# Kernel tuning notes

Hardware: AMD Instinct MI355X
Metric: run time of the kernel (lower is better)

The kernel has to match this reference:

```python
import jax, jax.numpy as jnp
import numpy as np

EPS = 1e-5
K_NN = 16

def _lin1d(x, W, b):
    # 1x1 Conv1d: x (B,C,N) -> (B,O,N)
    return jnp.einsum('oc,bcn->bon', W, x) + b[None, :, None]

def _lin2d(x, W, b):
    # 1x1 Conv2d: x (B,C,N,K) -> (B,O,N,K)
    return jnp.einsum('oc,bcnk->bonk', W, x) + b[None, :, None, None]

def _bn2d(x, gamma, beta):
    # train-mode BatchNorm2d over (B, N, K) per channel
    mean = jnp.mean(x, axis=(0, 2, 3), keepdims=True)
    var = jnp.var(x, axis=(0, 2, 3), keepdims=True)
    xh = (x - mean) * jax.lax.rsqrt(var + EPS)
    return gamma[None, :, None, None] * xh + beta[None, :, None, None]

def _knn_idx(pq, ps, k):
    # pq (B,3,N), ps (B,3,M) -> idx (B,N,K) of k nearest support points
    d2 = (jnp.sum(pq * pq, axis=1)[:, :, None]
          + jnp.sum(ps * ps, axis=1)[:, None, :]
          - 2.0 * jnp.einsum('bcn,bcm->bnm', pq, ps))
    _, idx = jax.lax.top_k(-d2, k)
    return idx

def _group(x, idx):
    # x (B,C,M), idx (B,N,K) -> (B,C,N,K)
    return jnp.take_along_axis(x[:, :, None, :], idx[:, None, :, :], axis=3)

def setup_inputs() -> dict:
    key = jax.random.key(0)
    ks = jax.random.split(key, 20)
    B, C, D, N, M, H = 4, 128, 64, 2048, 2048, 256
    s = lambda k, shape, scale: (jax.random.normal(k, shape, dtype=jnp.float32) * scale)
    return {
        'pq': s(ks[0], (B, 3, N), 1.0),
        'fq': s(ks[1], (B, C, N), 1.0),
        'ps': s(ks[2], (B, 3, M), 1.0),
        'fs': s(ks[3], (B, C, M), 1.0),
        'Wq': s(ks[4], (D, C), 0.05), 'bq': jnp.zeros((D,), jnp.float32),
        'Wk': s(ks[5], (D, C), 0.05), 'bk': jnp.zeros((D,), jnp.float32),
        'Wv': s(ks[6], (D, C), 0.05), 'bv': jnp.zeros((D,), jnp.float32),
        'Wp1': s(ks[7], (D, 3), 0.2), 'bp1': jnp.zeros((D,), jnp.float32),
        'gp': jnp.ones((D,), jnp.float32), 'btp': jnp.zeros((D,), jnp.float32),
        'Wp2': s(ks[8], (D, D), 0.05), 'bp2': jnp.zeros((D,), jnp.float32),
        'Wa1': s(ks[9], (H, D), 0.05), 'ba1': jnp.zeros((H,), jnp.float32),
        'ga': jnp.ones((H,), jnp.float32), 'bta': jnp.zeros((H,), jnp.float32),
        'Wa2': s(ks[10], (D, H), 0.05), 'ba2': jnp.zeros((D,), jnp.float32),
        'We': s(ks[11], (C, D), 0.05), 'be': jnp.zeros((C,), jnp.float32),
    }

def reference(pq, fq, ps, fs, Wq, bq, Wk, bk, Wv, bv,
              Wp1, bp1, gp, btp, Wp2, bp2,
              Wa1, ba1, ga, bta, Wa2, ba2, We, be):
    identity = fq
    q = _lin1d(fq, Wq, bq)          # (B,D,N)
    k = _lin1d(fs, Wk, bk)          # (B,D,M)
    v = _lin1d(fs, Wv, bv)          # (B,D,M)
    idx = _knn_idx(pq, ps, K_NN)    # (B,N,K)
    key_g = _group(k, idx)          # (B,D,N,K)
    qk_rel = q[:, :, :, None] - key_g
    pos_rel = pq[:, :, :, None] - _group(ps, idx)  # (B,3,N,K)
    # pos_mlp: conv-bn-relu-conv
    pe = _lin2d(pos_rel, Wp1, bp1)
    pe = jax.nn.relu(_bn2d(pe, gp, btp))
    pe = _lin2d(pe, Wp2, bp2)       # (B,D,N,K)
    # attn_mlp: conv-bn-relu-conv
    a = _lin2d(qk_rel + pe, Wa1, ba1)
    a = jax.nn.relu(_bn2d(a, ga, bta))
    a = _lin2d(a, Wa2, ba2)         # (B,D,N,K)
    attn = jax.nn.softmax(a, axis=-1)
    val = _group(v, idx) + pe       # (B,D,N,K)
    agg = jnp.einsum('bcnk,bcnk->bcn', attn, val)
    return _lin1d(agg, We, be) + identity
```

## Files before the change

kernel.cpp:

```cpp
#include <hip/hip_runtime.h>
#include <stdint.h>

#define NN 2048
#define MM 2048
#define NSAMP 131072

typedef float  fv4 __attribute__((ext_vector_type(4)));
typedef short  bfv8 __attribute__((ext_vector_type(8)));
typedef short  bfv4 __attribute__((ext_vector_type(4)));
typedef unsigned short u16;
typedef unsigned long long u64;

__device__ inline u16 f2bf(float x){
  unsigned u = __float_as_uint(x);
  return (u16)((u + 0x7FFFu + ((u>>16)&1u)) >> 16);
}
__device__ inline float bf2f(u16 u){ return __uint_as_float(((unsigned)u)<<16); }
__device__ inline bfv8 ld8f(const float* __restrict__ p){
  fv4 a = *(const fv4*)p;
  fv4 b = *(const fv4*)(p + 4);
  bfv8 r;
  r[0]=(short)f2bf(a.x); r[1]=(short)f2bf(a.y); r[2]=(short)f2bf(a.z); r[3]=(short)f2bf(a.w);
  r[4]=(short)f2bf(b.x); r[5]=(short)f2bf(b.y); r[6]=(short)f2bf(b.z); r[7]=(short)f2bf(b.w);
  return r;
}
#define MFMA16 __builtin_amdgcn_mfma_f32_16x16x32_bf16

__global__ __launch_bounds__(256) void k_front(
    const float* __restrict__ fq, const float* __restrict__ fs,
    const float* __restrict__ Wq, const float* __restrict__ Wk, const float* __restrict__ Wv,
    const float* __restrict__ bq, const float* __restrict__ bk, const float* __restrict__ bv,
    const float* __restrict__ pq, const float* __restrict__ ps,
    float* __restrict__ qT, float* __restrict__ kT, float* __restrict__ vT,
    int* __restrict__ idxb, float* __restrict__ posPart) {
  __shared__ __align__(16) unsigned char smem[17408];
  const int t = threadIdx.x;

  if (blockIdx.x < 256) {
    u16* tile = (u16*)smem;
    int bid = blockIdx.x;
    int b = bid >> 6, p0 = (bid & 63) * 32;
    int w = t >> 6, l = t & 63, lq = l >> 4, ln = l & 15;
    {
      int cq = t >> 3, n4 = (t & 7) * 4;
      #pragma unroll
      for (int it = 0; it < 4; ++it) {
        int c = it * 32 + cq;
        fv4 vq = *(const fv4*)&fq[(b*128 + c)*2048 + p0 + n4];
        fv4 vs = *(const fv4*)&fs[(b*128 + c)*2048 + p0 + n4];
        #pragma unroll
        for (int j = 0; j < 4; ++j) {
          tile[0*32*136 + (n4 + j)*136 + c] = f2bf(vq[j]);
          tile[1*32*136 + (n4 + j)*136 + c] = f2bf(vs[j]);
        }
      }
    }
    bfv8 A[3][4];
    #pragma unroll
    for (int mat = 0; mat < 3; ++mat) {
      const float* W = mat == 0 ? Wq : (mat == 1 ? Wk : Wv);
      #pragma unroll
      for (int kk = 0; kk < 4; ++kk)
        A[mat][kk] = ld8f(W + (w*16 + ln)*128 + kk*32 + lq*8);
    }
    __syncthreads();
    fv4 acc[3][2];
    #pragma unroll
    for (int mat = 0; mat < 3; ++mat) {
      const u16* tl = tile + (mat == 0 ? 0 : 32*136);
      #pragma unroll
      for (int nt = 0; nt < 2; ++nt) {
        fv4 a = {0.f,0.f,0.f,0.f};
        #pragma unroll
        for (int kk = 0; kk < 4; ++kk) {
          bfv8 bb = *(const bfv8*)&tl[(nt*16 + ln)*136 + kk*32 + lq*8];
          a = MFMA16(A[mat][kk], bb, a, 0, 0, 0);
        }
        acc[mat][nt] = a;
      }
    }
    #pragma unroll
    for (int mat = 0; mat < 3; ++mat) {
      float* dst = mat == 0 ? qT : (mat == 1 ? kT : vT);
      const float* bia = mat == 0 ? bq : (mat == 1 ? bk : bv);
      fv4 bq4 = *(const fv4*)&bia[w*16 + lq*4];
      #pragma unroll
      for (int nt = 0; nt < 2; ++nt) {
        fv4 o = acc[mat][nt] + bq4;
        *(fv4*)&dst[(b*NN + p0 + nt*16 + ln)*64 + w*16 + lq*4] = o;
      }
    }
    return;
  }

  u64*   list = (u64*)smem;
  u64*   win  = (u64*)(smem + 16384);
  int*   cnt  = (int*)(smem + 16896);
  float* sacc = (float*)(smem + 16912);

  const int kbid = blockIdx.x - 256;
  const int w = t >> 6, lane = t & 63;
  const int qi = kbid * 4 + w;
  const int b = qi >> 11, n = qi & 2047;
  const float* pqb = pq + b * 3 * NN;
  const float* psb = ps + b * 3 * MM;
  const float qx = pqb[n], qy = pqb[NN + n], qz = pqb[2 * NN + n];
  const float qq = qx * qx + qy * qy + qz * qz;

  unsigned key[32];
  unsigned bkey = 0xFFFFFFFFu; unsigned bj = 0;
  #pragma unroll
  for (int j = 0; j < 32; ++j) {
    int m = lane + 64*j;
    float x = psb[m], y = psb[MM + m], z = psb[2*MM + m];
    float w2 = x*x + y*y + z*z;
    float d2 = qq + w2 - 2.f * (qx * x + qy * y + qz * z);
    unsigned bu = __float_as_uint(d2);
    bu = (bu & 0x80000000u) ? ~bu : (bu | 0x80000000u);
    key[j] = bu;
    if (bu < bkey) { bkey = bu; bj = (unsigned)j; }
  }
  u64 e = (((u64)bkey) << 32) | (unsigned)(lane + 64*(int)bj);

  #pragma unroll
  for (int k = 2; k <= 64; k <<= 1) {
    #pragma unroll
    for (int j = k >> 1; j > 0; j >>= 1) {
      u64 x = __shfl_xor(e, j, 64);
      u64 lo = e < x ? e : x, hi = e < x ? x : e;
      bool up = ((lane & k) == 0);
      bool takeLo = (((lane & j) == 0) == up);
      e = takeLo ? lo : hi;
    }
  }
  const u64 thr = __shfl(e, 15, 64);
  const unsigned T32 = (unsigned)(thr >> 32);

  if (lane == 0) cnt[w] = 0;
  #pragma unroll
  for (int j = 0; j < 32; ++j) {
    if (key[j] <= T32) {
      int p = atomicAdd(&cnt[w], 1);
      if (p < 512) list[w*512 + p] = (((u64)key[j]) << 32) | (unsigned)(lane + 64*j);
    }
  }
  const int C = *(volatile int*)&cnt[w];

  u64 myWin = 0;
  if (C <= 64) {
    u64 v = (lane < C) ? list[w*512 + lane] : ~0ULL;
    #pragma unroll
    for (int k = 2; k <= 64; k <<= 1) {
      #pragma unroll
      for (int j = k >> 1; j > 0; j >>= 1) {
        u64 x = __shfl_xor(v, j, 64);
        u64 lo = v < x ? v : x, hi = v < x ? x : v;
        bool up = ((lane & k) == 0);
        bool takeLo = (((lane & j) == 0) == up);
        v = takeLo ? lo : hi;
      }
    }
    myWin = v;
  } else if (C <= 128) {
    u64 e0 = list[w*512 + lane];
    u64 e1 = (64 + lane < C) ? list[w*512 + 64 + lane] : ~0ULL;
    #pragma unroll
    for (unsigned k = 2; k <= 128; k <<= 1) {
      #pragma unroll
      for (unsigned j = k >> 1; j > 0; j >>= 1) {
        if (j < 64) {
          u64 x0 = __shfl_xor(e0, (int)j, 64);
          u64 x1 = __shfl_xor(e1, (int)j, 64);
          bool lower = ((lane & j) == 0);
          bool up0 = (k == 128) ? true : ((lane & k) == 0);
          bool up1 = (k == 128) ? true : ((k == 64) ? false : ((lane & k) == 0));
          e0 = (lower == up0) ? (e0 < x0 ? e0 : x0) : (e0 < x0 ? x0 : e0);
          e1 = (lower == up1) ? (e1 < x1 ? e1 : x1) : (e1 < x1 ? x1 : e1);
        } else {
          u64 lo = e0 < e1 ? e0 : e1, hi = e0 < e1 ? e1 : e0;
          e0 = lo; e1 = hi;
        }
      }
    }
    myWin = e0;
  } else {
    int Cc = C > 512 ? 512 : C;
    for (int i = lane; i < 512; i += 64)
      if (i >= Cc) list[w*512 + i] = ~0ULL;
    for (int r = 0; r < 16; ++r) {
      u64 mv = ~0ULL;
      #pragma unroll
      for (int s5 = 0; s5 < 8; ++s5) {
        u64 x = list[w*512 + s5*64 + lane];
        mv = x < mv ? x : mv;
      }
      #pragma unroll
      for (int off = 1; off <= 32; off <<= 1) {
        u64 x = __shfl_xor(mv, off, 64);
        mv = x < mv ? x : mv;
      }
      #pragma unroll
      for (int s5 = 0; s5 < 8; ++s5)
        if (list[w*512 + s5*64 + lane] == mv) list[w*512 + s5*64 + lane] = ~0ULL;
      if (lane == 0) win[w*16 + r] = mv;
    }
    if (lane < 16) myWin = win[w*16 + lane];
  }

  if (lane < 16) {
    unsigned m = (unsigned)(myWin & 0xFFFFFFFFu);
    idxb[qi * 16 + lane] = (int)m;
    float x = psb[m], y = psb[MM + m], z = psb[2*MM + m];
    float r0 = qx - x, r1 = qy - y, r2 = qz - z;
    float s[9];
    s[0] = r0; s[1] = r1; s[2] = r2;
    s[3] = r0*r0; s[4] = r0*r1; s[5] = r0*r2;
    s[6] = r1*r1; s[7] = r1*r2; s[8] = r2*r2;
    #pragma unroll
    for (int off = 1; off <= 8; off <<= 1)
      #pragma unroll
      for (int i = 0; i < 9; ++i) s[i] += __shfl_xor(s[i], off, 64);
    if (lane == 0)
      #pragma unroll
      for (int i = 0; i < 9; ++i) sacc[w*9 + i] = s[i];
  }
  __syncthreads();
  if (t < 9) posPart[kbid * 12 + t]
      = sacc[0*9 + t] + sacc[1*9 + t] + sacc[2*9 + t] + sacc[3*9 + t];
}

__global__ __launch_bounds__(256) void k_ystats(
    const float* __restrict__ pq, const float* __restrict__ ps,
    const float* __restrict__ qT, const float* __restrict__ kT,
    const int* __restrict__ idxb, const float* __restrict__ posPart,
    const float* __restrict__ Wp1, const float* __restrict__ bp1,
    const float* __restrict__ gp, const float* __restrict__ btp,
    const float* __restrict__ Wp2, const float* __restrict__ bp2,
    float* __restrict__ Wp1f, float* __restrict__ bp1f,
    float* __restrict__ Gpart, float* __restrict__ ySumPart) {
  __shared__ __align__(16) unsigned char smem[21760];
  u16*   hp   = (u16*)smem;
  u16*   y2   = (u16*)(smem + 9216);
  float* r3   = (float*)(smem + 18432);
  float* qc   = (float*)(smem + 19200);
  int*   idxA = (int*)(smem + 20224);
  float* sWp1 = (float*)(smem + 20480);
  float* sbp1 = (float*)(smem + 21248);
  float* sbp2 = (float*)(smem + 21504);

  const int t = threadIdx.x;
  const int w = t >> 6, l = t & 63, lq = l >> 4, ln = l & 15;
  const int d0 = 16*w + lq*4;

  if (t < 64) sbp2[t] = bp2[t];

  bfv8 Ape[2];
  #pragma unroll
  for (int kk = 0; kk < 2; ++kk)
    Ape[kk] = ld8f(Wp2 + (16*w + ln)*64 + kk*32 + lq*8);

  {
    float* red = r3;
    float* stf = r3 + 40;
    float s[9];
    #pragma unroll
    for (int i = 0; i < 9; ++i) s[i] = 0.f;
    #pragma unroll
    for (int it = 0; it < 8; ++it) {
      const float* p = posPart + (it * 256 + t) * 12;
      fv4 a = *(const fv4*)p;
      fv4 b4 = *(const fv4*)(p + 4);
      float c8 = p[8];
      s[0]+=a.x; s[1]+=a.y; s[2]+=a.z; s[3]+=a.w;
      s[4]+=b4.x; s[5]+=b4.y; s[6]+=b4.z; s[7]+=b4.w;
      s[8]+=c8;
    }
    #pragma unroll
    for (int off = 32; off > 0; off >>= 1)
      #pragma unroll
      for (int i = 0; i < 9; ++i) s[i] += __shfl_xor(s[i], off, 64);
    if (l == 0)
      #pragma unroll
      for (int i = 0; i < 9; ++i) red[w*9 + i] = s[i];
    __syncthreads();
    if (t < 9) stf[t] = red[0*9+t] + red[1*9+t] + red[2*9+t] + red[3*9+t];
    __syncthreads();
    if (t < 64) {
      int d = t;
      const float invN = 1.f / (float)NSAMP;
      float m0 = stf[0]*invN, m1 = stf[1]*invN, m2 = stf[2]*invN;
      float C00 = stf[3]*invN - m0*m0, C01 = stf[4]*invN - m0*m1, C02 = stf[5]*invN - m0*m2;
      float C11 = stf[6]*invN - m1*m1, C12 = stf[7]*invN - m1*m2, C22 = stf[8]*invN - m2*m2;
      float w0 = Wp1[d*3], w1 = Wp1[d*3+1], w2 = Wp1[d*3+2];
      float mean = w0*m0 + w1*m1 + w2*m2 + bp1[d];
      float var = w0*w0*C00 + w1*w1*C11 + w2*w2*C22 + 2.f*(w0*w1*C01 + w0*w2*C02 + w1*w2*C12);
      float scale = gp[d] * rsqrtf(var + 1e-5f);
      float wf0 = scale * w0, wf1 = scale * w1, wf2 = scale * w2;
      float bf = btp[d] + scale * (bp1[d] - mean);
      sWp1[d*3] = wf0; sWp1[d*3+1] = wf1; sWp1[d*3+2] = wf2;
      sbp1[d] = bf;
      if (blockIdx.x == 0) {
        Wp1f[d*3] = wf0; Wp1f[d*3+1] = wf1; Wp1f[d*3+2] = wf2;
        bp1f[d] = bf;
      }
    }
  }

  fv4 gacc[4];
  #pragma unroll
  for (int nt = 0; nt < 4; ++nt) gacc[nt] = (fv4){0.f,0.f,0.f,0.f};
  float ys[4] = {0.f, 0.f, 0.f, 0.f};
  __syncthreads();

  for (int ch = 0; ch < 4; ++ch) {
    const int p0 = blockIdx.x * 16 + ch * 4;
    const int b  = p0 >> 11;
    const int bN = b * 2048;
    if (t < 64) idxA[t] = idxb[p0*16 + t];
    qc[t] = qT[(p0 + (t>>6))*64 + (t & 63)];
    __syncthreads();
    if (t < 192) { int c = t >> 6, s = t & 63; int n = (p0 + (s>>4)) & 2047;
      r3[c*64 + s] = pq[(b*3+c)*NN + n] - ps[(b*3+c)*MM + idxA[s]]; }
    __syncthreads();
    { int s = t >> 2, iq = t & 3;
      float r0 = r3[s], r1 = r3[64+s], r2 = r3[128+s];
      u16 tmp[16];
      #pragma unroll
      for (int e = 0; e < 16; ++e) { int i = iq*16 + e;
        float v = sbp1[i] + sWp1[i*3]*r0 + sWp1[i*3+1]*r1 + sWp1[i*3+2]*r2;
        tmp[e] = f2bf(fmaxf(v, 0.f)); }
      *(bfv8*)&hp[s*72 + iq*16]     = *(const bfv8*)&tmp[0];
      *(bfv8*)&hp[s*72 + iq*16 + 8] = *(const bfv8*)&tmp[8];
    }
    __syncthreads();
    {
      fv4 pe[4];
      #pragma unroll
      for (int nt = 0; nt < 4; ++nt) {
        fv4 acc = {0.f,0.f,0.f,0.f};
        #pragma unroll
        for (int kk = 0; kk < 2; ++kk) {
          bfv8 bb = *(const bfv8*)&hp[(nt*16 + ln)*72 + kk*32 + lq*8];
          acc = MFMA16(Ape[kk], bb, acc, 0, 0, 0);
        }
        pe[nt] = acc;
      }
      fv4 bp2q = *(const fv4*)&sbp2[d0];
      #pragma unroll
      for (int nt = 0; nt < 4; ++nt) {
        int s = nt*16 + ln;
        int mi = idxA[s];
        fv4 kg = *(const fv4*)(kT + (bN + mi)*64 + d0);
        fv4 qv = *(const fv4*)&qc[nt*64 + d0];
        fv4 yv = qv - kg + pe[nt] + bp2q;
        #pragma unroll
        for (int r = 0; r < 4; ++r) { y2[(d0 + r)*72 + s] = f2bf(yv[r]); ys[r] += yv[r]; }
      }
    }
    __syncthreads();
    #pragma unroll
    for (int kk = 0; kk < 2; ++kk) {
      bfv8 aa = *(const bfv8*)&y2[(16*w + ln)*72 + kk*32 + lq*8];
      #pragma unroll
      for (int nt = 0; nt < 4; ++nt) {
        bfv8 bb = *(const bfv8*)&y2[(nt*16 + ln)*72 + kk*32 + lq*8];
        gacc[nt] = MFMA16(aa, bb, gacc[nt], 0, 0, 0);
      }
    }
    __syncthreads();
  }
  #pragma unroll
  for (int nt = 0; nt < 4; ++nt)
    #pragma unroll
    for (int r = 0; r < 4; ++r)
      Gpart[blockIdx.x*4096 + (16*w + lq*4 + r)*64 + nt*16 + ln] = gacc[nt][r];
  #pragma unroll
  for (int off = 1; off <= 8; off <<= 1) {
    #pragma unroll
    for (int r = 0; r < 4; ++r) ys[r] += __shfl_xor(ys[r], off, 64);
  }
  if (ln == 0) {
    #pragma unroll
    for (int r = 0; r < 4; ++r) ySumPart[blockIdx.x*64 + d0 + r] = ys[r];
  }
}

__global__ __launch_bounds__(256) void k_gred(
    const float* __restrict__ Gpart, const float* __restrict__ ySumPart,
    float* __restrict__ G, float* __restrict__ ySum) {
  __shared__ float red[256];
  int bid = blockIdx.x, t = threadIdx.x;
  int tj = t & 63, st = t >> 6;
  if (bid < 64) {
    int j = bid * 64 + tj;
    float s = 0.f;
    for (int p = st * 128; p < st * 128 + 128; ++p)
      s += Gpart[p*4096 + j];
    red[st * 64 + tj] = s;
    __syncthreads();
    if (t < 64)
      G[bid * 64 + t] = red[t] + red[64 + t] + red[128 + t] + red[192 + t];
  } else {
    float s = 0.f;
    for (int p = st * 128; p < st * 128 + 128; ++p)
      s += ySumPart[p*64 + tj];
    red[st * 64 + tj] = s;
    __syncthreads();
    if (t < 64)
      ySum[t] = red[t] + red[64 + t] + red[128 + t] + red[192 + t];
  }
}

__global__ __launch_bounds__(256) void k_attnfinal(
    const float* __restrict__ Wa1, const float* __restrict__ ba1,
    const float* __restrict__ ga, const float* __restrict__ bta,
    const float* __restrict__ ySum, const float* __restrict__ G,
    u16* __restrict__ Wa1fbf, float* __restrict__ ba1f) {
  __shared__ float red[256];
  __shared__ float mu[64];
  __shared__ float sc[1];
  int h = blockIdx.x, t = threadIdx.x;
  const float invN = 1.f / (float)NSAMP;
  if (t < 64) mu[t] = ySum[t] * invN;
  __syncthreads();
  float acc = 0.f;
  #pragma unroll
  for (int e = 0; e < 16; ++e) {
    int pi = t*16 + e, i = pi >> 6, j = pi & 63;
    float cov = G[pi]*invN - mu[i]*mu[j];
    acc += Wa1[h*64 + i] * Wa1[h*64 + j] * cov;
  }
  red[t] = acc;
  __syncthreads();
  for (int s = 128; s > 0; s >>= 1) { if (t < s) red[t] += red[t + s]; __syncthreads(); }
  float var = red[0];
  __syncthreads();
  red[t] = (t < 64) ? Wa1[h*64 + t] * mu[t] : 0.f;
  __syncthreads();
  for (int s = 128; s > 0; s >>= 1) { if (t < s) red[t] += red[t + s]; __syncthreads(); }
  if (t == 0) {
    float mean  = red[0] + ba1[h];
    float scale = ga[h] * rsqrtf(var + 1e-5f);
    sc[0] = scale;
    ba1f[h] = bta[h] + scale * (ba1[h] - mean);
  }
  __syncthreads();
  if (t < 64) Wa1fbf[h*64 + t] = f2bf(sc[0] * Wa1[h*64 + t]);
}

__global__ __launch_bounds__(256) void k_main(
    const float* __restrict__ pq, const float* __restrict__ ps,
    const float* __restrict__ qT, const float* __restrict__ kT, const float* __restrict__ vT,
    const int* __restrict__ idxb,
    const float* __restrict__ Wp1f, const float* __restrict__ bp1f,
    const float* __restrict__ Wp2, const float* __restrict__ bp2,
    const u16* __restrict__ Wa1fbf, const float* __restrict__ ba1f,
    const float* __restrict__ Wa2, const float* __restrict__ ba2,
    const float* __restrict__ We, const float* __restrict__ be,
    const float* __restrict__ fq,
    u16* __restrict__ aggbf, float* __restrict__ out) {
  __shared__ __align__(16) unsigned char smem[65024];
  u16*   hp   = (u16*)smem;
  u16*   ha   = (u16*)smem;
  u16*   ylds = (u16*)(smem + 33792);
  float* at   = (float*)(smem + 33792);
  u16*   vt   = (u16*)(smem + 51200);
  float* r3   = (float*)(smem + 60416);
  float* qc   = (float*)(smem + 61184);
  int*   idxA = (int*)(smem + 62208);
  float* sWp1 = (float*)(smem + 62464);
  float* sbp1 = (float*)(smem + 63232);
  float* sbp2 = (float*)(smem + 63488);
  float* sba1 = (float*)(smem + 63744);
  float* sba2 = (float*)(smem + 64768);

  const int t = threadIdx.x;
  const int w = t >> 6, l = t & 63, lq = l >> 4, ln = l & 15;
  const int d0 = 16*w + lq*4;

  if (t < 192) sWp1[t] = Wp1f[t];
  if (t < 64){ sbp1[t] = bp1f[t]; sbp2[t] = bp2[t]; sba2[t] = ba2[t]; }
  sba1[t] = ba1f[t];

  bfv8 Ape[2], A1[4][2], A2[8];
  #pragma unroll
  for (int kk = 0; kk < 2; ++kk)
    Ape[kk] = ld8f(Wp2 + (16*w + ln)*64 + kk*32 + lq*8);
  #pragma unroll
  for (int mt = 0; mt < 4; ++mt)
    #pragma unroll
    for (int kk = 0; kk < 2; ++kk)
      A1[mt][kk] = *(const bfv8*)(Wa1fbf + (64*w + mt*16 + ln)*64 + kk*32 + lq*8);
  #pragma unroll
  for (int kk = 0; kk < 8; ++kk)
    A2[kk] = ld8f(Wa2 + (16*w + ln)*256 + kk*32 + lq*8);
  __syncthreads();

  for (int ch = 0; ch < 4; ++ch) {
    const int p0 = blockIdx.x * 16 + ch * 4;
    const int b  = p0 >> 11;
    const int bN = b * 2048;
    if (t < 64) idxA[t] = idxb[p0*16 + t];
    qc[t] = qT[(p0 + (t>>6))*64 + (t & 63)];
    __syncthreads();
    if (t < 192) { int c = t >> 6, s = t & 63; int n = (p0 + (s>>4)) & 2047;
      r3[c*64 + s] = pq[(b*3+c)*NN + n] - ps[(b*3+c)*MM + idxA[s]]; }
    __syncthreads();
    { int s = t >> 2, iq = t & 3;
      float r0 = r3[s], r1 = r3[64+s], r2 = r3[128+s];
      u16 tmp[16];
      #pragma unroll
      for (int e = 0; e < 16; ++e) { int i = iq*16 + e;
        float v = sbp1[i] + sWp1[i*3]*r0 + sWp1[i*3+1]*r1 + sWp1[i*3+2]*r2;
        tmp[e] = f2bf(fmaxf(v, 0.f)); }
      *(bfv8*)&hp[s*72 + iq*16]     = *(const bfv8*)&tmp[0];
      *(bfv8*)&hp[s*72 + iq*16 + 8] = *(const bfv8*)&tmp[8];
    }
    __syncthreads();
    {
      fv4 pe[4];
      #pragma unroll
      for (int nt = 0; nt < 4; ++nt) {
        fv4 acc = {0.f,0.f,0.f,0.f};
        #pragma unroll
        for (int kk = 0; kk < 2; ++kk) {
          bfv8 bb = *(const bfv8*)&hp[(nt*16 + ln)*72 + kk*32 + lq*8];
          acc = MFMA16(Ape[kk], bb, acc, 0, 0, 0);
        }
        pe[nt] = acc;
      }
      fv4 bp2q = *(const fv4*)&sbp2[d0];
      #pragma unroll
      for (int nt = 0; nt < 4; ++nt) {
        int s = nt*16 + ln;
        int mi = idxA[s];
        fv4 kg = *(const fv4*)(kT + (bN + mi)*64 + d0);
        fv4 vg = *(const fv4*)(vT + (bN + mi)*64 + d0);
        fv4 qv = *(const fv4*)&qc[nt*64 + d0];
        fv4 pv = pe[nt] + bp2q;
        fv4 yv = qv - kg + pv;
        fv4 vv = vg + pv;
        u16 yp[4], vp[4];
        #pragma unroll
        for (int r = 0; r < 4; ++r) { yp[r] = f2bf(yv[r]); vp[r] = f2bf(vv[r]); }
        *(bfv4*)&ylds[s*72 + d0] = *(const bfv4*)yp;
        *(bfv4*)&vt[s*72 + d0]   = *(const bfv4*)vp;
      }
    }
    __syncthreads();
    #pragma unroll
    for (int nt = 0; nt < 4; ++nt) {
      int s = nt*16 + ln;
      bfv8 b0 = *(const bfv8*)&ylds[s*72 + lq*8];
      bfv8 b1 = *(const bfv8*)&ylds[s*72 + 32 + lq*8];
      #pragma unroll
      for (int mt = 0; mt < 4; ++mt) {
        fv4 acc = {0.f,0.f,0.f,0.f};
        acc = MFMA16(A1[mt][0], b0, acc, 0, 0, 0);
        acc = MFMA16(A1[mt][1], b1, acc, 0, 0, 0);
        int h0 = 64*w + mt*16 + lq*4;
        fv4 bq = *(const fv4*)&sba1[h0];
        u16 hv[4];
        #pragma unroll
        for (int r = 0; r < 4; ++r) hv[r] = f2bf(fmaxf(acc[r] + bq[r], 0.f));
        *(bfv4*)&ha[s*264 + h0] = *(const bfv4*)hv;
      }
    }
    __syncthreads();
    {
      fv4 acc2[4];
      #pragma unroll
      for (int nt = 0; nt < 4; ++nt) acc2[nt] = (fv4){0.f,0.f,0.f,0.f};
      #pragma unroll
      for (int kk = 0; kk < 8; ++kk) {
        #pragma unroll
        for (int nt = 0; nt < 4; ++nt) {
          bfv8 bb = *(const bfv8*)&ha[(nt*16 + ln)*264 + kk*32 + lq*8];
          acc2[nt] = MFMA16(A2[kk], bb, acc2[nt], 0, 0, 0);
        }
      }
      fv4 ba2q = *(const fv4*)&sba2[d0];
      #pragma unroll
      for (int nt = 0; nt < 4; ++nt) {
        int s = nt*16 + ln;
        fv4 o = acc2[nt] + ba2q;
        *(fv4*)&at[s*68 + d0] = o;
      }
    }
    __syncthreads();
    {
      int dd = t & 63, pt = t >> 6;
      float a[16];
      #pragma unroll
      for (int k = 0; k < 16; ++k) a[k] = at[(pt*16 + k)*68 + dd];
      float mx = a[0];
      #pragma unroll
      for (int k = 1; k < 16; ++k) mx = fmaxf(mx, a[k]);
      float sum = 0.f, num = 0.f;
      #pragma unroll
      for (int k = 0; k < 16; ++k) {
        float e = __expf(a[k] - mx);
        sum += e;
        num += e * bf2f(vt[(pt*16 + k)*72 + dd]);
      }
      aggbf[(p0 + pt)*64 + dd] = f2bf(num / sum);
    }
    __syncthreads();
  }
  {
    const int P0 = blockIdx.x * 16;
    const int b  = P0 >> 11;
    const int n0 = P0 & 2047;
    bfv8 EA[2][2];
    #pragma unroll
    for (int mt = 0; mt < 2; ++mt)
      #pragma unroll
      for (int kk = 0; kk < 2; ++kk)
        EA[mt][kk] = ld8f(We + ((w*2 + mt)*16 + ln)*64 + kk*32 + lq*8);
    const u16* bp = aggbf + (P0 + ln)*64;
    bfv8 b0 = *(const bfv8*)(bp + lq*8);
    bfv8 b1 = *(const bfv8*)(bp + 32 + lq*8);
    fv4 eacc[2];
    #pragma unroll
    for (int mt = 0; mt < 2; ++mt) {
      fv4 a = {0.f,0.f,0.f,0.f};
      a = MFMA16(EA[mt][0], b0, a, 0, 0, 0);
      a = MFMA16(EA[mt][1], b1, a, 0, 0, 0);
      eacc[mt] = a;
    }
    #pragma unroll
    for (int mt = 0; mt < 2; ++mt) {
      int c0 = (w*2 + mt)*16 + lq*4;
      fv4 bev = *(const fv4*)&be[c0];
      #pragma unroll
      for (int r = 0; r < 4; ++r) {
        int c = c0 + r;
        int o = (b*128 + c)*2048 + n0 + ln;
        out[o] = eacc[mt][r] + bev[r] + fq[o];
      }
    }
  }
}

extern "C" void kernel_launch(void* const* d_in, const int* in_sizes, int n_in,
                              void* d_out, int out_size, void* d_ws, size_t ws_size,
                              hipStream_t stream) {
  (void)in_sizes; (void)n_in; (void)out_size; (void)ws_size;
  const float* pq  = (const float*)d_in[0];
  const float* fq  = (const float*)d_in[1];
  const float* ps  = (const float*)d_in[2];
  const float* fs  = (const float*)d_in[3];
  const float* Wq  = (const float*)d_in[4];  const float* bq  = (const float*)d_in[5];
  const float* Wk  = (const float*)d_in[6];  const float* bk  = (const float*)d_in[7];
  const float* Wv  = (const float*)d_in[8];  const float* bv  = (const float*)d_in[9];
  const float* Wp1 = (const float*)d_in[10]; const float* bp1 = (const float*)d_in[11];
  const float* gp  = (const float*)d_in[12]; const float* btp = (const float*)d_in[13];
  const float* Wp2 = (const float*)d_in[14]; const float* bp2 = (const float*)d_in[15];
  const float* Wa1 = (const float*)d_in[16]; const float* ba1 = (const float*)d_in[17];
  const float* ga  = (const float*)d_in[18]; const float* bta = (const float*)d_in[19];
  const float* Wa2 = (const float*)d_in[20]; const float* ba2 = (const float*)d_in[21];
  const float* We  = (const float*)d_in[22]; const float* be  = (const float*)d_in[23];
  float* ws = (float*)d_ws;
  float* qT    = ws;
  float* kT    = ws + 524288;
  float* vT    = ws + 1048576;
  u16*   aggbf = (u16*)(ws + 1572864);
  int*   idxb  = (int*)(ws + 1835008);
  float* Wp1f  = ws + 1998848;
  float* bp1f  = ws + 1999040;
  float* ba1f  = ws + 1999104;
  float* G     = ws + 1999360;
  float* ySum  = ws + 2003456;
  float* ySumP = ws + 2003520;
  u16*   Wa1fbf = (u16*)(ws + 2036288);
  float* posPart = ws + 2044480;
  float* Gpart   = ws + 2069056;
  float* out   = (float*)d_out;

  k_front<<<2304, 256, 0, stream>>>(fq, fs, Wq, Wk, Wv, bq, bk, bv, pq, ps,
                                    qT, kT, vT, idxb, posPart);
  k_ystats<<<512, 256, 0, stream>>>(pq, ps, qT, kT, idxb, posPart,
                                    Wp1, bp1, gp, btp, Wp2, bp2,
                                    Wp1f, bp1f, Gpart, ySumP);
  k_gred<<<65, 256, 0, stream>>>(Gpart, ySumP, G, ySum);
  k_attnfinal<<<256, 256, 0, stream>>>(Wa1, ba1, ga, bta, ySum, G, Wa1fbf, ba1f);
  k_main<<<512, 256, 0, stream>>>(pq, ps, qT, kT, vT, idxb, Wp1f, bp1f, Wp2, bp2,
                                  Wa1fbf, ba1f, Wa2, ba2, We, be, fq, aggbf, out);
}
```

Measured before the change: 208.6 us.

## Compute attn BN stats directly from Wa1·y instead of covariance Gram matrix

The ystats kernel now multiplies each tile of y by Wa1 with MFMA and accumulates per-channel sums and sums of squares of the 256 pre-BN attention channels. This replaces the 64x64 Gram-matrix partials, so the k_gred reduction kernel and the covariance contraction in k_attnfinal go away. That removes one launch and the large Gpart write and read traffic, at the cost of more MFMA work and registers in ystats. The variance now comes from E[a²]-E[a]² over bf16 MFMA outputs, which may change numerical accuracy.

```diff
diff --git a/kernel.cpp b/kernel.cpp
--- a/kernel.cpp
+++ b/kernel.cpp
@@ -236,11 +236,12 @@
     const float* __restrict__ Wp1, const float* __restrict__ bp1,
     const float* __restrict__ gp, const float* __restrict__ btp,
     const float* __restrict__ Wp2, const float* __restrict__ bp2,
+    const float* __restrict__ Wa1,
     float* __restrict__ Wp1f, float* __restrict__ bp1f,
-    float* __restrict__ Gpart, float* __restrict__ ySumPart) {
+    float* __restrict__ aSumP, float* __restrict__ aSqP) {
   __shared__ __align__(16) unsigned char smem[21760];
   u16*   hp   = (u16*)smem;
-  u16*   y2   = (u16*)(smem + 9216);
+  u16*   ylds = (u16*)(smem + 9216);
   float* r3   = (float*)(smem + 18432);
   float* qc   = (float*)(smem + 19200);
   int*   idxA = (int*)(smem + 20224);
@@ -254,10 +255,15 @@
 
   if (t < 64) sbp2[t] = bp2[t];
 
-  bfv8 Ape[2];
+  bfv8 Ape[2], A1[4][2];
   #pragma unroll
   for (int kk = 0; kk < 2; ++kk)
     Ape[kk] = ld8f(Wp2 + (16*w + ln)*64 + kk*32 + lq*8);
+  #pragma unroll
+  for (int mt = 0; mt < 4; ++mt)
+    #pragma unroll
+    for (int kk = 0; kk < 2; ++kk)
+      A1[mt][kk] = ld8f(Wa1 + (64*w + mt*16 + ln)*64 + kk*32 + lq*8);
 
   {
     float* red = r3;
@@ -306,10 +312,9 @@
     }
   }
 
-  fv4 gacc[4];
-  #pragma unroll
-  for (int nt = 0; nt < 4; ++nt) gacc[nt] = (fv4){0.f,0.f,0.f,0.f};
-  float ys[4] = {0.f, 0.f, 0.f, 0.f};
+  float aS[16], aQ[16];
+  #pragma unroll
+  for (int i = 0; i < 16; ++i) { aS[i] = 0.f; aQ[i] = 0.f; }
   __syncthreads();
 
   for (int ch = 0; ch < 4; ++ch) {
@@ -353,93 +358,74 @@
         fv4 kg = *(const fv4*)(kT + (bN + mi)*64 + d0);
         fv4 qv = *(const fv4*)&qc[nt*64 + d0];
         fv4 yv = qv - kg + pe[nt] + bp2q;
-        #pragma unroll
-        for (int r = 0; r < 4; ++r) { y2[(d0 + r)*72 + s] = f2bf(yv[r]); ys[r] += yv[r]; }
-      }
-    }
-    __syncthreads();
-    #pragma unroll
-    for (int kk = 0; kk < 2; ++kk) {
-      bfv8 aa = *(const bfv8*)&y2[(16*w + ln)*72 + kk*32 + lq*8];
-      #pragma unroll
-      for (int nt = 0; nt < 4; ++nt) {
-        bfv8 bb = *(const bfv8*)&y2[(nt*16 + ln)*72 + kk*32 + lq*8];
-        gacc[nt] = MFMA16(aa, bb, gacc[nt], 0, 0, 0);
-      }
-    }
-    __syncthreads();
-  }
-  #pragma unroll
-  for (int nt = 0; nt < 4; ++nt)
-    #pragma unroll
-    for (int r = 0; r < 4; ++r)
-      Gpart[blockIdx.x*4096 + (16*w + lq*4 + r)*64 + nt*16 + ln] = gacc[nt][r];
-  #pragma unroll
-  for (int off = 1; off <= 8; off <<= 1) {
-    #pragma unroll
-    for (int r = 0; r < 4; ++r) ys[r] += __shfl_xor(ys[r], off, 64);
-  }
+        u16 yp[4];
+        #pragma unroll
+        for (int r = 0; r < 4; ++r) yp[r] = f2bf(yv[r]);
+        *(bfv4*)&ylds[s*72 + d0] = *(const bfv4*)yp;
+      }
+    }
+    __syncthreads();
+    #pragma unroll
+    for (int nt = 0; nt < 4; ++nt) {
+      int s = nt*16 + ln;
+      bfv8 yb0 = *(const bfv8*)&ylds[s*72 + lq*8];
+      bfv8 yb1 = *(const bfv8*)&ylds[s*72 + 32 + lq*8];
+      #pragma unroll
+      for (int mt = 0; mt < 4; ++mt) {
+        fv4 acc = {0.f,0.f,0.f,0.f};
+        acc = MFMA16(A1[mt][0], yb0, acc, 0, 0, 0);
+        acc = MFMA16(A1[mt][1], yb1, acc, 0, 0, 0);
+        #pragma unroll
+        for (int r = 0; r < 4; ++r) {
+          float a = acc[r];
+          aS[mt*4 + r] += a;
+          aQ[mt*4 + r] += a * a;
+        }
+      }
+    }
+    __syncthreads();
+  }
+  #pragma unroll
+  for (int off = 1; off <= 8; off <<= 1)
+    #pragma unroll
+    for (int i = 0; i < 16; ++i) {
+      aS[i] += __shfl_xor(aS[i], off, 16);
+      aQ[i] += __shfl_xor(aQ[i], off, 16);
+    }
   if (ln == 0) {
     #pragma unroll
-    for (int r = 0; r < 4; ++r) ySumPart[blockIdx.x*64 + d0 + r] = ys[r];
-  }
-}
-
-__global__ __launch_bounds__(256) void k_gred(
-    const float* __restrict__ Gpart, const float* __restrict__ ySumPart,
-    float* __restrict__ G, float* __restrict__ ySum) {
-  __shared__ float red[256];
-  int bid = blockIdx.x, t = threadIdx.x;
-  int tj = t & 63, st = t >> 6;
-  if (bid < 64) {
-    int j = bid * 64 + tj;
-    float s = 0.f;
-    for (int p = st * 128; p < st * 128 + 128; ++p)
-      s += Gpart[p*4096 + j];
-    red[st * 64 + tj] = s;
-    __syncthreads();
-    if (t < 64)
-      G[bid * 64 + t] = red[t] + red[64 + t] + red[128 + t] + red[192 + t];
-  } else {
-    float s = 0.f;
-    for (int p = st * 128; p < st * 128 + 128; ++p)
-      s += ySumPart[p*64 + tj];
-    red[st * 64 + tj] = s;
-    __syncthreads();
-    if (t < 64)
-      ySum[t] = red[t] + red[64 + t] + red[128 + t] + red[192 + t];
+    for (int mt = 0; mt < 4; ++mt)
+      #pragma unroll
+      for (int r = 0; r < 4; ++r) {
+        int h = 64*w + mt*16 + lq*4 + r;
+        aSumP[h*512 + blockIdx.x] = aS[mt*4 + r];
+        aSqP[h*512 + blockIdx.x]  = aQ[mt*4 + r];
+      }
   }
 }
 
 __global__ __launch_bounds__(256) void k_attnfinal(
     const float* __restrict__ Wa1, const float* __restrict__ ba1,
     const float* __restrict__ ga, const float* __restrict__ bta,
-    const float* __restrict__ ySum, const float* __restrict__ G,
+    const float* __restrict__ aSumP, const float* __restrict__ aSqP,
     u16* __restrict__ Wa1fbf, float* __restrict__ ba1f) {
-  __shared__ float red[256];
-  __shared__ float mu[64];
+  __shared__ float redS[256];
+  __shared__ float redQ[256];
   __shared__ float sc[1];
   int h = blockIdx.x, t = threadIdx.x;
-  const float invN = 1.f / (float)NSAMP;
-  if (t < 64) mu[t] = ySum[t] * invN;
+  float S = aSumP[h*512 + t] + aSumP[h*512 + 256 + t];
+  float Q = aSqP[h*512 + t]  + aSqP[h*512 + 256 + t];
+  redS[t] = S; redQ[t] = Q;
   __syncthreads();
-  float acc = 0.f;
-  #pragma unroll
-  for (int e = 0; e < 16; ++e) {
-    int pi = t*16 + e, i = pi >> 6, j = pi & 63;
-    float cov = G[pi]*invN - mu[i]*mu[j];
-    acc += Wa1[h*64 + i] * Wa1[h*64 + j] * cov;
-  }
-  red[t] = acc;
-  __syncthreads();
-  for (int s = 128; s > 0; s >>= 1) { if (t < s) red[t] += red[t + s]; __syncthreads(); }
-  float var = red[0];
-  __syncthreads();
-  red[t] = (t < 64) ? Wa1[h*64 + t] * mu[t] : 0.f;
-  __syncthreads();
-  for (int s = 128; s > 0; s >>= 1) { if (t < s) red[t] += red[t + s]; __syncthreads(); }
+  for (int s = 128; s > 0; s >>= 1) {
+    if (t < s) { redS[t] += redS[t + s]; redQ[t] += redQ[t + s]; }
+    __syncthreads();
+  }
   if (t == 0) {
-    float mean  = red[0] + ba1[h];
+    const float invN = 1.f / (float)NSAMP;
+    float m   = redS[0] * invN;
+    float var = redQ[0] * invN - m * m;
+    float mean  = m + ba1[h];
     float scale = ga[h] * rsqrtf(var + 1e-5f);
     sc[0] = scale;
     ba1f[h] = bta[h] + scale * (ba1[h] - mean);
@@ -669,21 +655,19 @@
   float* Wp1f  = ws + 1998848;
   float* bp1f  = ws + 1999040;
   float* ba1f  = ws + 1999104;
-  float* G     = ws + 1999360;
-  float* ySum  = ws + 2003456;
-  float* ySumP = ws + 2003520;
-  u16*   Wa1fbf = (u16*)(ws + 2036288);
-  float* posPart = ws + 2044480;
-  float* Gpart   = ws + 2069056;
+  u16*   Wa1fbf = (u16*)(ws + 1999360);
+  float* posPart = ws + 2007552;
+  float* aSumP  = ws + 2032128;
+  float* aSqP   = ws + 2163200;
   float* out   = (float*)d_out;
 
   k_front<<<2304, 256, 0, stream>>>(fq, fs, Wq, Wk, Wv, bq, bk, bv, pq, ps,
                                     qT, kT, vT, idxb, posPart);
   k_ystats<<<512, 256, 0, stream>>>(pq, ps, qT, kT, idxb, posPart,
-                                    Wp1, bp1, gp, btp, Wp2, bp2,
-                                    Wp1f, bp1f, Gpart, ySumP);
-  k_gred<<<65, 256, 0, stream>>>(Gpart, ySumP, G, ySum);
-  k_attnfinal<<<256, 256, 0, stream>>>(Wa1, ba1, ga, bta, ySum, G, Wa1fbf, ba1f);
+                                    Wp1, bp1, gp, btp, Wp2, bp2, Wa1,
+                                    Wp1f, bp1f, aSumP, aSqP);
+  k_attnfinal<<<256, 256, 0, stream>>>(Wa1, ba1, ga, bta, aSumP, aSqP,
+                                       Wa1fbf, ba1f);
   k_main<<<512, 256, 0, stream>>>(pq, ps, qT, kT, vT, idxb, Wp1f, bp1f, Wp2, bp2,
                                   Wa1fbf, ba1f, Wa2, ba2, We, be, fq, aggbf, out);
 }
```

New measurement: 210.3 us. About the same (+0.8%).
